# Performance work log

Hardware: AMD Instinct MI355X
Metric: run time of the kernel (lower is better)

## Reference

```python
import jax, jax.numpy as jnp
import numpy as np

Q, L = 512, 4096


def setup_inputs() -> dict:
    key = jax.random.key(0)
    ks = jax.random.split(key, 12)
    def rn(k, shape, s=0.05):
        return jax.random.normal(k, shape, jnp.float32) * s
    return {
        "reactions": jax.random.normal(ks[0], (1, Q, 256), jnp.float32),
        "protein":   jax.random.normal(ks[1], (1, L, 1024), jnp.float32),
        # conv1d(1024->256, k=1) == pointwise linear
        "Wc":  rn(ks[2], (256, 1024)), "bc":  jnp.zeros((256,), jnp.float32),
        "W1":  rn(ks[3], (64, 256)),   "b1":  jnp.zeros((64,), jnp.float32),
        "W2":  rn(ks[4], (64, 256)),   "b2":  jnp.zeros((64,), jnp.float32),
        "Wa":  rn(ks[5], (64, 64)),    "ba":  jnp.zeros((64,), jnp.float32),
        "Wpa": rn(ks[6], (64, 64)),    "bpa": jnp.zeros((64,), jnp.float32),
        "Wra": rn(ks[7], (64, 64)),    "bra": jnp.zeros((64,), jnp.float32),
        "Wf1": rn(ks[8], (256, 128)),  "bf1": jnp.zeros((256,), jnp.float32),
        "Wf2": rn(ks[9], (128, 256)),  "bf2": jnp.zeros((128,), jnp.float32),
        "Wf3": rn(ks[10], (1, 128)),   "bf3": jnp.zeros((1,), jnp.float32),
    }


def reference(reactions, protein, Wc, bc, W1, b1, W2, b2, Wa, ba,
              Wpa, bpa, Wra, bra, Wf1, bf1, Wf2, bf2, Wf3, bf3):
    # protein: [1, L, 1024] -> 1x1 conv over channels == linear -> [L, 256]
    p = jax.nn.relu(protein[0] @ Wc.T + bc)
    # reactions: [1, Q, 256] -> [Q, 64]
    r = jax.nn.relu(reactions[0] @ W2.T + b2)
    # protein tokens -> [L, 64]
    k = jax.nn.relu(p @ W1.T + b1)

    ra = r @ Wra.T + bra            # [Q, 64]
    pa = k @ Wpa.T + bpa            # [L, 64]
    # broadcast outer-sum + relu + small linear: [Q, L, 64]
    A = jax.nn.relu(ra[:, None, :] + pa[None, :, :]) @ Wa.T + ba

    r_gate = jax.nn.sigmoid(jnp.mean(A, axis=1))   # [Q, 64]
    p_gate = jax.nn.sigmoid(jnp.mean(A, axis=0))   # [L, 64]

    rxnfp = r + r * r_gate                          # [Q, 64]
    prot = jnp.max(k + k * p_gate, axis=0)          # [64]  maxpool over L

    ctx = jnp.concatenate(
        [rxnfp, jnp.broadcast_to(prot, (rxnfp.shape[0], 64))], axis=1)  # [Q,128]

    # dropout layers are identity in eval mode
    h = jax.nn.leaky_relu(ctx @ Wf1.T + bf1)
    h = jax.nn.leaky_relu(h @ Wf2.T + bf2)
    out = h @ Wf3.T + bf3
    return out.reshape(-1)                          # [Q]
```

## Files before the change

### kernel.cpp

```cpp
#include <hip/hip_runtime.h>
#include <hip/hip_bf16.h>
#include <math.h>

#define TPB 256

typedef __attribute__((ext_vector_type(8))) short s16x8;
typedef __attribute__((ext_vector_type(4))) float f32x4;

#define MFMA16(a, b, c) __builtin_amdgcn_mfma_f32_16x16x32_bf16((a), (b), (c), 0, 0, 0)

constexpr unsigned OFF_P    = 0u;
constexpr unsigned OFF_K    = OFF_P    + 4096u*256u;
constexpr unsigned OFF_PA   = OFF_K    + 4096u*64u;
constexpr unsigned OFF_R    = OFF_PA   + 4096u*64u;
constexpr unsigned OFF_RA   = OFF_R    + 512u*64u;
constexpr unsigned OFF_SR   = OFF_RA   + 512u*64u;
constexpr unsigned OFF_PMAX = OFF_SR   + 512u*64u;
constexpr unsigned OFF_SP   = OFF_PMAX + 64u;
constexpr unsigned OFF_PAT  = OFF_SP   + 4096u*64u;
constexpr unsigned OFF_RAT  = OFF_PAT  + 64u*4096u;
constexpr unsigned OFF_ABF  = OFF_RAT  + 64u*512u;
constexpr unsigned OFF_WBF  = OFF_ABF  + 2097152u;

__device__ __forceinline__ short f2bf(float x) {
  union { float f; unsigned u; } v; v.f = x;
  unsigned r = v.u + 0x7FFFu + ((v.u >> 16) & 1u);
  return (short)(r >> 16);
}
__device__ __forceinline__ unsigned pkbf(float a, float b) {
  __hip_bfloat162 h = __float22bfloat162_rn(make_float2(a, b));
  union { __hip_bfloat162 h2; unsigned u; } v; v.h2 = h;
  return v.u;
}
union U8 { s16x8 s; unsigned u[4]; };

__global__ __launch_bounds__(TPB) void k0_cvt(
    const float* __restrict__ prot, const float* __restrict__ Wc,
    float* __restrict__ ws)
{
  int bid = blockIdx.x, tid = threadIdx.x;
  if (bid >= 2176) {
    if (tid < 16)
      *(float4*)&ws[OFF_PMAX + tid * 4] = make_float4(0.f, 0.f, 0.f, 0.f);
    return;
  }
  const float* src; short* dst; size_t idx;
  if (bid < 2048) {
    src = prot; dst = (short*)(ws + OFF_ABF);
    idx = (size_t)bid * 2048 + (size_t)tid * 8;
  } else {
    src = Wc;   dst = (short*)(ws + OFF_WBF);
    idx = (size_t)(bid - 2048) * 2048 + (size_t)tid * 8;
  }
  float4 f0 = *(const float4*)(src + idx);
  float4 f1 = *(const float4*)(src + idx + 4);
  U8 s;
  s.u[0] = pkbf(f0.x, f0.y); s.u[1] = pkbf(f0.z, f0.w);
  s.u[2] = pkbf(f1.x, f1.y); s.u[3] = pkbf(f1.z, f1.w);
  *(s16x8*)(dst + idx) = s.s;
}

__global__ __launch_bounds__(TPB) void k1_gemm(
    const float* __restrict__ bc, float* __restrict__ ws)
{
  __shared__ __align__(16) short Asm[64 * 136];
  __shared__ __align__(16) short Bsm[64 * 136];
  int bid = blockIdx.x, tid = threadIdx.x;
  int m0 = (bid >> 2) * 64, n0 = (bid & 3) * 64;
  int wave = tid >> 6, lane = tid & 63;
  int lm = lane & 15, quad = lane >> 4;
  int wm = (wave & 1) * 32, wn = (wave >> 1) * 32;

  const short* Abf = (const short*)(ws + OFF_ABF);
  const short* Wbf = (const short*)(ws + OFF_WBF);
  int srow = tid >> 2, sc = (tid & 3) * 32;
  const short* Ag = Abf + (size_t)(m0 + srow) * 1024 + sc;
  const short* Bg = Wbf + (size_t)(n0 + srow) * 1024 + sc;

  s16x8 ar[4], br[4];
#pragma unroll
  for (int i = 0; i < 4; ++i) {
    ar[i] = *(const s16x8*)(Ag + i * 8);
    br[i] = *(const s16x8*)(Bg + i * 8);
  }

  f32x4 acc[2][2] = {};

  for (int kc = 0; kc < 8; ++kc) {
    __syncthreads();
#pragma unroll
    for (int i = 0; i < 4; ++i) {
      *(s16x8*)&Asm[srow * 136 + sc + i * 8] = ar[i];
      *(s16x8*)&Bsm[srow * 136 + sc + i * 8] = br[i];
    }
    if (kc < 7) {
#pragma unroll
      for (int i = 0; i < 4; ++i) {
        ar[i] = *(const s16x8*)(Ag + (kc + 1) * 128 + i * 8);
        br[i] = *(const s16x8*)(Bg + (kc + 1) * 128 + i * 8);
      }
    }
    __syncthreads();
#pragma unroll
    for (int ks = 0; ks < 4; ++ks) {
      s16x8 a0 = *(const s16x8*)&Asm[(wm + lm)      * 136 + ks * 32 + quad * 8];
      s16x8 a1 = *(const s16x8*)&Asm[(wm + 16 + lm) * 136 + ks * 32 + quad * 8];
      s16x8 b0 = *(const s16x8*)&Bsm[(wn + lm)      * 136 + ks * 32 + quad * 8];
      s16x8 b1 = *(const s16x8*)&Bsm[(wn + 16 + lm) * 136 + ks * 32 + quad * 8];
      acc[0][0] = MFMA16(a0, b0, acc[0][0]);
      acc[0][1] = MFMA16(a0, b1, acc[0][1]);
      acc[1][0] = MFMA16(a1, b0, acc[1][0]);
      acc[1][1] = MFMA16(a1, b1, acc[1][1]);
    }
  }

#pragma unroll
  for (int mi = 0; mi < 2; ++mi)
#pragma unroll
    for (int ni = 0; ni < 2; ++ni) {
      int col = n0 + wn + ni * 16 + lm;
      float bcv = bc[col];
#pragma unroll
      for (int r = 0; r < 4; ++r) {
        int row = m0 + wm + mi * 16 + quad * 4 + r;
        ws[OFF_P + (unsigned)row * 256u + col] = fmaxf(acc[mi][ni][r] + bcv, 0.f);
      }
    }
}

__global__ __launch_bounds__(TPB, 2) void k2_heads(
    const float* __restrict__ reactions,
    const float* __restrict__ W1,  const float* __restrict__ b1,
    const float* __restrict__ W2,  const float* __restrict__ b2,
    const float* __restrict__ Wpa, const float* __restrict__ bpa,
    const float* __restrict__ Wra, const float* __restrict__ bra,
    float* __restrict__ ws)
{
  __shared__ __align__(16) short Asm[32 * 264];
  __shared__ __align__(16) short Bsm[64 * 264];
  __shared__ __align__(16) short Ksm[32 * 72];
  __shared__ __align__(16) short Wsm[64 * 72];
  int bid = blockIdx.x, tid = threadIdx.x;
  bool isProt = bid < 128;
  int row0 = (isProt ? bid : (bid - 128)) * 32;
  const float* src  = isProt ? (ws + OFF_P) : reactions;
  const float* Wst1 = isProt ? W1 : W2;
  const float* bv   = isProt ? b1 : b2;
  const float* Wst2 = isProt ? Wpa : Wra;
  const float* b2nd = isProt ? bpa : bra;
  float* out1  = ws + (isProt ? OFF_K : OFF_R);
  float* out2T = ws + (isProt ? OFF_PAT : OFF_RAT);
  unsigned tstride = isProt ? 4096u : 512u;

  {
    int row = tid >> 3, seg = (tid & 7) * 32;
    const float* sp = src + (size_t)(row0 + row) * 256 + seg;
    float4 f[8];
#pragma unroll
    for (int i = 0; i < 8; ++i) f[i] = *(const float4*)(sp + i * 4);
#pragma unroll
    for (int i = 0; i < 4; ++i) {
      U8 s;
      s.u[0] = pkbf(f[2*i].x,   f[2*i].y);
      s.u[1] = pkbf(f[2*i].z,   f[2*i].w);
      s.u[2] = pkbf(f[2*i+1].x, f[2*i+1].y);
      s.u[3] = pkbf(f[2*i+1].z, f[2*i+1].w);
      *(s16x8*)&Asm[row * 264 + seg + i * 8] = s.s;
    }
  }
  {
    int row = tid >> 2, seg = (tid & 3) * 64;
    const float* sp = Wst1 + (size_t)row * 256 + seg;
#pragma unroll
    for (int i = 0; i < 8; ++i) {
      float4 fa = *(const float4*)(sp + i * 8);
      float4 fb = *(const float4*)(sp + i * 8 + 4);
      U8 s;
      s.u[0] = pkbf(fa.x, fa.y); s.u[1] = pkbf(fa.z, fa.w);
      s.u[2] = pkbf(fb.x, fb.y); s.u[3] = pkbf(fb.z, fb.w);
      *(s16x8*)&Bsm[row * 264 + seg + i * 8] = s.s;
    }
  }
  {
    int row = tid >> 2, seg = (tid & 3) * 16;
    const float* sp = Wst2 + (size_t)row * 64 + seg;
#pragma unroll
    for (int i = 0; i < 2; ++i) {
      float4 fa = *(const float4*)(sp + i * 8);
      float4 fb = *(const float4*)(sp + i * 8 + 4);
      U8 s;
      s.u[0] = pkbf(fa.x, fa.y); s.u[1] = pkbf(fa.z, fa.w);
      s.u[2] = pkbf(fb.x, fb.y); s.u[3] = pkbf(fb.z, fb.w);
      *(s16x8*)&Wsm[row * 72 + seg + i * 8] = s.s;
    }
  }
  __syncthreads();

  int wave = tid >> 6, lane = tid & 63;
  int lm = lane & 15, quad = lane >> 4;
  int wm = (wave >> 1) * 16, wn = (wave & 1) * 32;

  f32x4 acc[2] = {};
#pragma unroll
  for (int kc = 0; kc < 8; ++kc) {
    s16x8 a = *(const s16x8*)&Asm[(wm + lm) * 264 + kc * 32 + quad * 8];
#pragma unroll
    for (int ni = 0; ni < 2; ++ni) {
      s16x8 b = *(const s16x8*)&Bsm[(wn + ni * 16 + lm) * 264 + kc * 32 + quad * 8];
      acc[ni] = MFMA16(a, b, acc[ni]);
    }
  }
#pragma unroll
  for (int ni = 0; ni < 2; ++ni) {
    int col = wn + ni * 16 + lm;
    float bb = bv[col];
#pragma unroll
    for (int r = 0; r < 4; ++r) {
      int row = wm + quad * 4 + r;
      float kv = fmaxf(acc[ni][r] + bb, 0.f);
      out1[(size_t)(row0 + row) * 64 + col] = kv;
      Ksm[row * 72 + col] = f2bf(kv);
    }
  }
  __syncthreads();

  f32x4 acc2[2] = {};
#pragma unroll
  for (int kc = 0; kc < 2; ++kc) {
    s16x8 a = *(const s16x8*)&Ksm[(wm + lm) * 72 + kc * 32 + quad * 8];
#pragma unroll
    for (int ni = 0; ni < 2; ++ni) {
      s16x8 b = *(const s16x8*)&Wsm[(wn + ni * 16 + lm) * 72 + kc * 32 + quad * 8];
      acc2[ni] = MFMA16(a, b, acc2[ni]);
    }
  }
#pragma unroll
  for (int ni = 0; ni < 2; ++ni) {
    int col = wn + ni * 16 + lm;
    float bb = b2nd[col];
#pragma unroll
    for (int r = 0; r < 4; ++r) {
      int row = wm + quad * 4 + r;
      float v = acc2[ni][r] + bb;
      out2T[(size_t)col * tstride + (row0 + row)] = v;
    }
  }
}

__global__ __launch_bounds__(TPB) void k3h_hist(float* __restrict__ ws)
{
  __shared__ float xcol[4096];
  __shared__ float rcol[512];
  __shared__ float hc[1025];
  __shared__ float hs[1025];
  __shared__ float rmn[4], rmx[4];
  int bid = blockIdx.x, tid = threadIdx.x;
  int wave = tid >> 6, lane = tid & 63;
  bool passA = bid < 64;
  int c = passA ? bid : (bid - 64);
  const float* paT = ws + OFF_PAT + (size_t)c * 4096;
  const float* raT = ws + OFF_RAT + (size_t)c * 512;

  for (int i = tid * 4; i < 4096; i += TPB * 4)
    *(float4*)&xcol[i] = *(const float4*)(paT + i);
  if (tid * 4 < 512)
    *(float4*)&rcol[tid * 4] = *(const float4*)(raT + tid * 4);
  for (int i = tid; i < 1025; i += TPB) { hc[i] = 0.f; hs[i] = 0.f; }
  __syncthreads();

  const float* hsrc = passA ? xcol : rcol;
  int hn = passA ? 4096 : 512;
  float mn = 1e30f, mx = -1e30f;
  for (int i = tid; i < hn; i += TPB) {
    float x = hsrc[i];
    mn = fminf(mn, x); mx = fmaxf(mx, x);
  }
#pragma unroll
  for (int off = 32; off > 0; off >>= 1) {
    mn = fminf(mn, __shfl_down(mn, off));
    mx = fmaxf(mx, __shfl_down(mx, off));
  }
  if (lane == 0) { rmn[wave] = mn; rmx[wave] = mx; }
  __syncthreads();
  mn = fminf(fminf(rmn[0], rmn[1]), fminf(rmn[2], rmn[3]));
  mx = fmaxf(fmaxf(rmx[0], rmx[1]), fmaxf(rmx[2], rmx[3]));
  float w = (mx - mn) * (1.f / 1024.f);
  float invw = (w > 1e-30f) ? 1.f / w : 0.f;
  for (int i = tid; i < hn; i += TPB) {
    float x = hsrc[i];
    int b = (int)((x - mn) * invw);
    b = b < 0 ? 0 : (b > 1023 ? 1023 : b);
    atomicAdd(&hc[b], 1.f);
    atomicAdd(&hs[b], x);
  }
  __syncthreads();
  if (wave == 0) {
    float vc[16], vs[16], sc = 0.f, ss = 0.f;
#pragma unroll
    for (int i = 0; i < 16; ++i) {
      vc[i] = hc[lane * 16 + i]; sc += vc[i];
      vs[i] = hs[lane * 16 + i]; ss += vs[i];
    }
    float tc = sc, ts = ss;
#pragma unroll
    for (int off = 1; off < 64; off <<= 1) {
      float oc = __shfl_down(tc, off);
      float os = __shfl_down(ts, off);
      if (lane + off < 64) { tc += oc; ts += os; }
    }
    float runc = tc - sc, runs = ts - ss;
#pragma unroll
    for (int i = 15; i >= 0; --i) {
      runc += vc[i]; hc[lane * 16 + i] = runc;
      runs += vs[i]; hs[lane * 16 + i] = runs;
    }
  }
  __syncthreads();

  if (passA) {
    for (int q = tid; q < 512; q += TPB) {
      float u = rcol[q];
      float thr = -u;
      int b;
      if (thr < mn) b = 0;
      else { b = (int)((thr - mn) * invw) + 1; b = b > 1024 ? 1024 : b; }
      ws[OFF_SR + (unsigned)q * 64u + c] = u * hc[b] + hs[b];
    }
  } else {
    for (int l = tid; l < 4096; l += TPB) {
      float v = xcol[l];
      float thr = -v;
      int b;
      if (thr < mn) b = 0;
      else { b = (int)((thr - mn) * invw) + 1; b = b > 1024 ? 1024 : b; }
      ws[OFF_SP + (unsigned)l * 64u + c] = v * hc[b] + hs[b];
    }
  }
}

__global__ __launch_bounds__(TPB) void k3b_gate(
    const float* __restrict__ Wa, const float* __restrict__ ba,
    float* __restrict__ ws)
{
  __shared__ float sp[16 * 64];
  __shared__ float wat[64 * 65];
  int bid = blockIdx.x, tid = threadIdx.x;
  int c = tid & 63, g = tid >> 6;
  int l0 = bid * 16;
  {
    int idx = tid * 4;
    float4 v = *(const float4*)&ws[OFF_SP + (unsigned)l0 * 64u + idx];
    v.x *= (1.f / 512.f); v.y *= (1.f / 512.f);
    v.z *= (1.f / 512.f); v.w *= (1.f / 512.f);
    *(float4*)&sp[idx] = v;
  }
  for (int it = 0; it < 16; ++it) {
    int idx = it * TPB + tid;
    wat[(idx & 63) * 65 + (idx >> 6)] = Wa[idx];
  }
  __syncthreads();
  float vmax = 0.f;
  float bac = ba[c];
#pragma unroll
  for (int i = 0; i < 4; ++i) {
    int ll = g * 4 + i;
    float dot = 0.f;
#pragma unroll 8
    for (int jj = 0; jj < 64; ++jj)
      dot += sp[ll * 64 + jj] * wat[jj * 65 + c];
    float pg = 1.f / (1.f + __expf(-(dot + bac)));
    float val = ws[OFF_K + (unsigned)(l0 + ll) * 64u + c] * (1.f + pg);
    vmax = fmaxf(vmax, val);
  }
  atomicMax((int*)&ws[OFF_PMAX + c], __float_as_int(vmax));
}

__global__ __launch_bounds__(TPB) void k4_final(
    const float* __restrict__ Wa,  const float* __restrict__ ba,
    const float* __restrict__ Wf1, const float* __restrict__ bf1,
    const float* __restrict__ Wf2, const float* __restrict__ bf2,
    const float* __restrict__ Wf3, const float* __restrict__ bf3,
    float* __restrict__ ws, float* __restrict__ out)
{
  __shared__ __align__(16) short mrb[16 * 72];
  __shared__ __align__(16) short wab[64 * 72];
  __shared__ __align__(16) short ctxb[16 * 136];
  __shared__ __align__(16) short h1b[16 * 264];
  __shared__ __align__(16) short wgt[256 * 136];
  __shared__ float red[64];
  int bid = blockIdx.x, tid = threadIdx.x;
  int q0 = bid * 16;
  int wave = tid >> 6, lane = tid & 63;
  int lm = lane & 15, quad = lane >> 4;

  {
    int q = tid >> 4, c4 = (tid & 15) * 4;
    float4 v = *(const float4*)&ws[OFF_SR + (unsigned)(q0 + q) * 64u + c4];
    uint2 st = make_uint2(pkbf(v.x * (1.f/4096.f), v.y * (1.f/4096.f)),
                          pkbf(v.z * (1.f/4096.f), v.w * (1.f/4096.f)));
    *(uint2*)&mrb[q * 72 + c4] = st;
  }
#pragma unroll
  for (int it = 0; it < 4; ++it) {
    int i4 = it * TPB + tid;
    int row = i4 >> 4, c4 = (i4 & 15) * 4;
    float4 v = *(const float4*)&Wa[row * 64 + c4];
    uint2 st = make_uint2(pkbf(v.x, v.y), pkbf(v.z, v.w));
    *(uint2*)&wab[row * 72 + c4] = st;
  }
  __syncthreads();

  f32x4 gacc = {};
#pragma unroll
  for (int kc = 0; kc < 2; ++kc) {
    s16x8 a = *(const s16x8*)&mrb[lm * 72 + kc * 32 + quad * 8];
    s16x8 b = *(const s16x8*)&wab[(wave * 16 + lm) * 72 + kc * 32 + quad * 8];
    gacc = MFMA16(a, b, gacc);
  }
  {
    int c = wave * 16 + lm;
    float bac = ba[c];
    short pb = f2bf(ws[OFF_PMAX + c]);
#pragma unroll
    for (int r = 0; r < 4; ++r) {
      int q = quad * 4 + r;
      float gg = 1.f / (1.f + __expf(-(gacc[r] + bac)));
      float rv = ws[OFF_R + (unsigned)(q0 + q) * 64u + c];
      ctxb[q * 136 + c]      = f2bf(rv * (1.f + gg));
      ctxb[q * 136 + 64 + c] = pb;
    }
  }
#pragma unroll 4
  for (int it = 0; it < 32; ++it) {
    int i4 = it * TPB + tid;
    int row = i4 >> 5, c4 = (i4 & 31) * 4;
    float4 v = *(const float4*)&Wf1[row * 128 + c4];
    uint2 st = make_uint2(pkbf(v.x, v.y), pkbf(v.z, v.w));
    *(uint2*)&wgt[row * 136 + c4] = st;
  }
  __syncthreads();

  f32x4 h[4] = {};
#pragma unroll
  for (int kc = 0; kc < 4; ++kc) {
    s16x8 a = *(const s16x8*)&ctxb[lm * 136 + kc * 32 + quad * 8];
#pragma unroll
    for (int nt = 0; nt < 4; ++nt) {
      s16x8 b = *(const s16x8*)&wgt[(wave * 64 + nt * 16 + lm) * 136 + kc * 32 + quad * 8];
      h[nt] = MFMA16(a, b, h[nt]);
    }
  }
#pragma unroll
  for (int nt = 0; nt < 4; ++nt) {
    int n = wave * 64 + nt * 16 + lm;
    float bb = bf1[n];
#pragma unroll
    for (int r = 0; r < 4; ++r) {
      int q = quad * 4 + r;
      float v = h[nt][r] + bb;
      v = v > 0.f ? v : 0.01f * v;
      h1b[q * 264 + n] = f2bf(v);
    }
  }
  __syncthreads();

#pragma unroll 4
  for (int it = 0; it < 32; ++it) {
    int i4 = it * TPB + tid;
    int row = i4 >> 6, c4 = (i4 & 63) * 4;
    float4 v = *(const float4*)&Wf2[row * 256 + c4];
    uint2 st = make_uint2(pkbf(v.x, v.y), pkbf(v.z, v.w));
    *(uint2*)&wgt[row * 264 + c4] = st;
  }
  __syncthreads();

  f32x4 o[2] = {};
#pragma unroll
  for (int kc = 0; kc < 8; ++kc) {
    s16x8 a = *(const s16x8*)&h1b[lm * 264 + kc * 32 + quad * 8];
#pragma unroll
    for (int nt = 0; nt < 2; ++nt) {
      s16x8 b = *(const s16x8*)&wgt[(wave * 32 + nt * 16 + lm) * 264 + kc * 32 + quad * 8];
      o[nt] = MFMA16(a, b, o[nt]);
    }
  }
  float pv[4] = {0.f, 0.f, 0.f, 0.f};
#pragma unroll
  for (int nt = 0; nt < 2; ++nt) {
    int m = wave * 32 + nt * 16 + lm;
    float bb = bf2[m], w3 = Wf3[m];
#pragma unroll
    for (int r = 0; r < 4; ++r) {
      float v = o[nt][r] + bb;
      v = v > 0.f ? v : 0.01f * v;
      pv[r] += v * w3;
    }
  }
#pragma unroll
  for (int msk = 1; msk < 16; msk <<= 1)
#pragma unroll
    for (int r = 0; r < 4; ++r) pv[r] += __shfl_xor(pv[r], msk);
  if (lm == 0) {
#pragma unroll
    for (int r = 0; r < 4; ++r) red[(quad * 4 + r) * 4 + wave] = pv[r];
  }
  __syncthreads();
  if (tid < 16)
    out[q0 + tid] = red[tid * 4] + red[tid * 4 + 1] + red[tid * 4 + 2] +
                    red[tid * 4 + 3] + bf3[0];
}

extern "C" void kernel_launch(void* const* d_in, const int* in_sizes, int n_in,
                              void* d_out, int out_size, void* d_ws, size_t ws_size,
                              hipStream_t stream)
{
  const float* reactions = (const float*)d_in[0];
  const float* protein   = (const float*)d_in[1];
  const float* Wc  = (const float*)d_in[2];
  const float* bc  = (const float*)d_in[3];
  const float* W1  = (const float*)d_in[4];
  const float* b1  = (const float*)d_in[5];
  const float* W2  = (const float*)d_in[6];
  const float* b2  = (const float*)d_in[7];
  const float* Wa  = (const float*)d_in[8];
  const float* ba  = (const float*)d_in[9];
  const float* Wpa = (const float*)d_in[10];
  const float* bpa = (const float*)d_in[11];
  const float* Wra = (const float*)d_in[12];
  const float* bra = (const float*)d_in[13];
  const float* Wf1 = (const float*)d_in[14];
  const float* bf1 = (const float*)d_in[15];
  const float* Wf2 = (const float*)d_in[16];
  const float* bf2 = (const float*)d_in[17];
  const float* Wf3 = (const float*)d_in[18];
  const float* bf3 = (const float*)d_in[19];
  float* ws  = (float*)d_ws;
  float* out = (float*)d_out;

  hipLaunchKernelGGL(k0_cvt, dim3(2177), dim3(TPB), 0, stream,
                     protein, Wc, ws);
  hipLaunchKernelGGL(k1_gemm, dim3(256), dim3(TPB), 0, stream,
                     bc, ws);
  hipLaunchKernelGGL(k2_heads, dim3(144), dim3(TPB), 0, stream,
                     reactions, W1, b1, W2, b2, Wpa, bpa, Wra, bra, ws);
  hipLaunchKernelGGL(k3h_hist, dim3(128), dim3(TPB), 0, stream, ws);
  hipLaunchKernelGGL(k3b_gate, dim3(256), dim3(TPB), 0, stream, Wa, ba, ws);
  hipLaunchKernelGGL(k4_final, dim3(32), dim3(TPB), 0, stream,
                     Wa, ba, Wf1, bf1, Wf2, bf2, Wf3, bf3, ws, out);
}
```

Before: 170.7 us.

## Store conv output as bf16 and coalesce transposed intermediate writes

The conv stage now writes its ReLU output P directly as bf16 into a new workspace region. The heads kernel copies it straight into shared memory with no float-to-bf16 conversion, which halves the traffic for that intermediate. The transposed pa/ra outputs are staged through a padded shared-memory tile so they can be written as coalesced float4 stores. The histogram kernel's SR/SP outputs are switched to a channel-major layout so its stores become contiguous, and the gate and final kernels read them back transposed.

```diff
diff --git a/kernel.cpp b/kernel.cpp
--- a/kernel.cpp
+++ b/kernel.cpp
@@ -9,17 +9,15 @@
 
 #define MFMA16(a, b, c) __builtin_amdgcn_mfma_f32_16x16x32_bf16((a), (b), (c), 0, 0, 0)
 
-constexpr unsigned OFF_P    = 0u;
-constexpr unsigned OFF_K    = OFF_P    + 4096u*256u;
-constexpr unsigned OFF_PA   = OFF_K    + 4096u*64u;
-constexpr unsigned OFF_R    = OFF_PA   + 4096u*64u;
-constexpr unsigned OFF_RA   = OFF_R    + 512u*64u;
-constexpr unsigned OFF_SR   = OFF_RA   + 512u*64u;
-constexpr unsigned OFF_PMAX = OFF_SR   + 512u*64u;
-constexpr unsigned OFF_SP   = OFF_PMAX + 64u;
-constexpr unsigned OFF_PAT  = OFF_SP   + 4096u*64u;
+constexpr unsigned OFF_K    = 0u;
+constexpr unsigned OFF_R    = OFF_K    + 4096u*64u;
+constexpr unsigned OFF_SRT  = OFF_R    + 512u*64u;
+constexpr unsigned OFF_PMAX = OFF_SRT  + 64u*512u;
+constexpr unsigned OFF_SPT  = OFF_PMAX + 64u;
+constexpr unsigned OFF_PAT  = OFF_SPT  + 64u*4096u;
 constexpr unsigned OFF_RAT  = OFF_PAT  + 64u*4096u;
-constexpr unsigned OFF_ABF  = OFF_RAT  + 64u*512u;
+constexpr unsigned OFF_PBF  = OFF_RAT  + 64u*512u;
+constexpr unsigned OFF_ABF  = OFF_PBF  + 524288u;
 constexpr unsigned OFF_WBF  = OFF_ABF  + 2097152u;
 
 __device__ __forceinline__ short f2bf(float x) {
@@ -114,6 +112,7 @@
     }
   }
 
+  short* P = (short*)(ws + OFF_PBF);
 #pragma unroll
   for (int mi = 0; mi < 2; ++mi)
 #pragma unroll
@@ -123,7 +122,7 @@
 #pragma unroll
       for (int r = 0; r < 4; ++r) {
         int row = m0 + wm + mi * 16 + quad * 4 + r;
-        ws[OFF_P + (unsigned)row * 256u + col] = fmaxf(acc[mi][ni][r] + bcv, 0.f);
+        P[(unsigned)row * 256u + col] = f2bf(fmaxf(acc[mi][ni][r] + bcv, 0.f));
       }
     }
 }
@@ -140,10 +139,10 @@
   __shared__ __align__(16) short Bsm[64 * 264];
   __shared__ __align__(16) short Ksm[32 * 72];
   __shared__ __align__(16) short Wsm[64 * 72];
+  __shared__ float ftrans[64 * 33];
   int bid = blockIdx.x, tid = threadIdx.x;
   bool isProt = bid < 128;
   int row0 = (isProt ? bid : (bid - 128)) * 32;
-  const float* src  = isProt ? (ws + OFF_P) : reactions;
   const float* Wst1 = isProt ? W1 : W2;
   const float* bv   = isProt ? b1 : b2;
   const float* Wst2 = isProt ? Wpa : Wra;
@@ -152,9 +151,16 @@
   float* out2T = ws + (isProt ? OFF_PAT : OFF_RAT);
   unsigned tstride = isProt ? 4096u : 512u;
 
-  {
+  if (isProt) {
     int row = tid >> 3, seg = (tid & 7) * 32;
-    const float* sp = src + (size_t)(row0 + row) * 256 + seg;
+    const short* sp = (const short*)(ws + OFF_PBF) +
+                      (size_t)(row0 + row) * 256 + seg;
+#pragma unroll
+    for (int i = 0; i < 4; ++i)
+      *(s16x8*)&Asm[row * 264 + seg + i * 8] = *(const s16x8*)(sp + i * 8);
+  } else {
+    int row = tid >> 3, seg = (tid & 7) * 32;
+    const float* sp = reactions + (size_t)(row0 + row) * 256 + seg;
     float4 f[8];
 #pragma unroll
     for (int i = 0; i < 8; ++i) f[i] = *(const float4*)(sp + i * 4);
@@ -241,9 +247,19 @@
 #pragma unroll
     for (int r = 0; r < 4; ++r) {
       int row = wm + quad * 4 + r;
-      float v = acc2[ni][r] + bb;
-      out2T[(size_t)col * tstride + (row0 + row)] = v;
-    }
+      ftrans[col * 33 + row] = acc2[ni][r] + bb;
+    }
+  }
+  __syncthreads();
+  {
+    int colc = tid >> 2, seg = (tid & 3) * 8;
+    float t0 = ftrans[colc * 33 + seg + 0], t1 = ftrans[colc * 33 + seg + 1];
+    float t2 = ftrans[colc * 33 + seg + 2], t3 = ftrans[colc * 33 + seg + 3];
+    float t4 = ftrans[colc * 33 + seg + 4], t5 = ftrans[colc * 33 + seg + 5];
+    float t6 = ftrans[colc * 33 + seg + 6], t7 = ftrans[colc * 33 + seg + 7];
+    float* dp = out2T + (size_t)colc * tstride + row0 + seg;
+    *(float4*)dp       = make_float4(t0, t1, t2, t3);
+    *(float4*)(dp + 4) = make_float4(t4, t5, t6, t7);
   }
 }
 
@@ -324,7 +340,7 @@
       int b;
       if (thr < mn) b = 0;
       else { b = (int)((thr - mn) * invw) + 1; b = b > 1024 ? 1024 : b; }
-      ws[OFF_SR + (unsigned)q * 64u + c] = u * hc[b] + hs[b];
+      ws[OFF_SRT + (unsigned)c * 512u + q] = u * hc[b] + hs[b];
     }
   } else {
     for (int l = tid; l < 4096; l += TPB) {
@@ -333,7 +349,7 @@
       int b;
       if (thr < mn) b = 0;
       else { b = (int)((thr - mn) * invw) + 1; b = b > 1024 ? 1024 : b; }
-      ws[OFF_SP + (unsigned)l * 64u + c] = v * hc[b] + hs[b];
+      ws[OFF_SPT + (unsigned)c * 4096u + l] = v * hc[b] + hs[b];
     }
   }
 }
@@ -348,11 +364,12 @@
   int c = tid & 63, g = tid >> 6;
   int l0 = bid * 16;
   {
-    int idx = tid * 4;
-    float4 v = *(const float4*)&ws[OFF_SP + (unsigned)l0 * 64u + idx];
-    v.x *= (1.f / 512.f); v.y *= (1.f / 512.f);
-    v.z *= (1.f / 512.f); v.w *= (1.f / 512.f);
-    *(float4*)&sp[idx] = v;
+    int cc = tid >> 2, part = tid & 3;
+    float4 v = *(const float4*)&ws[OFF_SPT + (unsigned)cc * 4096u + l0 + part * 4];
+    sp[(part * 4 + 0) * 64 + cc] = v.x * (1.f / 512.f);
+    sp[(part * 4 + 1) * 64 + cc] = v.y * (1.f / 512.f);
+    sp[(part * 4 + 2) * 64 + cc] = v.z * (1.f / 512.f);
+    sp[(part * 4 + 3) * 64 + cc] = v.w * (1.f / 512.f);
   }
   for (int it = 0; it < 16; ++it) {
     int idx = it * TPB + tid;
@@ -394,11 +411,12 @@
   int lm = lane & 15, quad = lane >> 4;
 
   {
-    int q = tid >> 4, c4 = (tid & 15) * 4;
-    float4 v = *(const float4*)&ws[OFF_SR + (unsigned)(q0 + q) * 64u + c4];
-    uint2 st = make_uint2(pkbf(v.x * (1.f/4096.f), v.y * (1.f/4096.f)),
-                          pkbf(v.z * (1.f/4096.f), v.w * (1.f/4096.f)));
-    *(uint2*)&mrb[q * 72 + c4] = st;
+    int cc = tid >> 2, part = tid & 3;
+    float4 v = *(const float4*)&ws[OFF_SRT + (unsigned)cc * 512u + q0 + part * 4];
+    mrb[(part * 4 + 0) * 72 + cc] = f2bf(v.x * (1.f / 4096.f));
+    mrb[(part * 4 + 1) * 72 + cc] = f2bf(v.y * (1.f / 4096.f));
+    mrb[(part * 4 + 2) * 72 + cc] = f2bf(v.z * (1.f / 4096.f));
+    mrb[(part * 4 + 3) * 72 + cc] = f2bf(v.w * (1.f / 4096.f));
   }
 #pragma unroll
   for (int it = 0; it < 4; ++it) {
```

Result: no change. 168.1 us (-1.5%).
